# Performance work log

Hardware: AMD Instinct MI355X
Metric: run time of the kernel (lower is better)

Reference implementation:

```python
import jax, jax.numpy as jnp
import numpy as np

B, T = 16, 8192
L, RC, DC, SC, EC, E, NC = 16, 32, 32, 256, 256, 100, 256


def conv1d(x, w, b, dilation=1):
    # x: [B, Cin, T], w: [Cout, Cin, K], b: [Cout]
    y = jax.lax.conv_general_dilated(
        x, w, window_strides=(1,), padding='VALID',
        rhs_dilation=(dilation,), dimension_numbers=('NCH', 'OIH', 'NCH'))
    return y + b[None, :, None]


def setup_inputs() -> dict:
    key = jax.random.key(0)
    ks = jax.random.split(key, 32)
    n = lambda k, shp: (jax.random.normal(k, shp) * 0.1).astype(jnp.float32)
    return dict(
        tokens=jax.random.randint(ks[0], (B, T), 0, NC),
        emb=n(ks[1], (NC, E)),
        init_w=n(ks[2], (RC, E, 1)), init_b=n(ks[3], (RC,)),
        dil_w=n(ks[4], (L, DC, RC, 2)), dil_b=n(ks[5], (L, DC)),
        filt_w=n(ks[6], (L, DC, DC, 2)), filt_b=n(ks[7], (L, DC)),
        gate_w=n(ks[8], (L, DC, DC, 2)), gate_b=n(ks[9], (L, DC)),
        res_w=n(ks[10], (L, RC, DC, 1)), res_b=n(ks[11], (L, RC)),
        skip_w=n(ks[12], (L, SC, DC, 1)), skip_b=n(ks[13], (L, SC)),
        end1_w=n(ks[14], (EC, SC, 1)), end1_b=n(ks[15], (EC,)),
        end2_w=n(ks[16], (EC, EC, 1)), end2_b=n(ks[17], (EC,)),
        fc1_w=n(ks[18], (128, 256)), fc1_b=n(ks[19], (128,)),
        fc2_w=n(ks[20], (128, 128)), fc2_b=n(ks[21], (128,)),
        fc3_w=n(ks[22], (64, 128)), fc3_b=n(ks[23], (64,)),
        fc4_w=n(ks[24], (NC, 64)), fc4_b=n(ks[25], (NC,)),
    )


def reference(tokens, emb, init_w, init_b, dil_w, dil_b, filt_w, filt_b,
              gate_w, gate_b, res_w, res_b, skip_w, skip_b,
              end1_w, end1_b, end2_w, end2_b,
              fc1_w, fc1_b, fc2_w, fc2_b, fc3_w, fc3_b, fc4_w, fc4_b):
    x = emb[tokens]                     # [B, T, E]
    x = jnp.transpose(x, (0, 2, 1))     # [B, E, T]
    x = conv1d(x, init_w, init_b)       # [B, RC, T]
    skip = None
    for i in range(L):
        d = 2 ** (i % 4)                # dilation resets each block of 4 layers
        xp = jnp.pad(x, ((0, 0), (0, 0), (d + 1, 0)))        # left pad d+1
        residual = conv1d(xp, dil_w[i], dil_b[i], dilation=d)  # [B, DC, T+1]
        f = jnp.tanh(conv1d(residual, filt_w[i], filt_b[i]))   # [B, DC, T]
        g = jax.nn.sigmoid(conv1d(residual, gate_w[i], gate_b[i]))
        x = f * g
        skip = conv1d(x, skip_w[i], skip_b[i])   # overwritten each layer (source bug, kept faithful)
        x = conv1d(x, res_w[i], res_b[i]) + residual[:, :, :-1]
    h = jax.nn.relu(conv1d(jax.nn.relu(skip), end1_w, end1_b))
    h = conv1d(h, end2_w, end2_b)       # [B, EC, T]
    h = h[:, :, -1]                     # [B, 256] last timestep only
    h = jax.nn.relu(h @ fc1_w.T + fc1_b)
    h = jax.nn.relu(h @ fc2_w.T + fc2_b)
    h = jax.nn.relu(h @ fc3_w.T + fc3_b)
    out = h @ fc4_w.T + fc4_b           # [B, NC]
    return out
```

## Files before the change

### kernel.cpp

```cpp
#include <hip/hip_runtime.h>


#define BB 16
#define TT 8192
#define LL 16
#define W0 77
#define NT 256

typedef __attribute__((ext_vector_type(8)))  short short8;
typedef __attribute__((ext_vector_type(16))) float float16;

#define MFMA_B16(a, b, c) __builtin_amdgcn_mfma_f32_32x32x16_bf16(a, b, c, 0, 0, 0)

__device__ __forceinline__ short f2bs(float f) {
  union { float ff; unsigned u; } v; v.ff = f;
  unsigned u = v.u;
  return (short)((u + 0x7FFFu + ((u >> 16) & 1u)) >> 16);
}
__device__ __forceinline__ float b2f(short h) {
  union { unsigned u; float f; } v;
  v.u = ((unsigned)(unsigned short)h) << 16; return v.f;
}
__device__ __forceinline__ float fast_sigmoid(float x) {
  return 1.f / (1.f + __expf(-x));
}
__device__ __forceinline__ float fast_tanh(float x) {
  return 2.f / (1.f + __expf(-2.f * x)) - 1.f;
}

__device__ __forceinline__ void bfrag2(const float* w, int n, int kh, short8* out) {
  #pragma unroll
  for (int h = 0; h < 2; h++) {
    short8 v;
    #pragma unroll
    for (int j = 0; j < 8; j++) v[j] = f2bs(w[(16 * h + kh * 8 + j) * 32 + n]);
    out[h] = v;
  }
}
__device__ __forceinline__ void afrag2(const short* src, int row, int kh, short8* out) {
  #pragma unroll
  for (int h = 0; h < 2; h++)
    out[h] = *(const short8*)&src[row * 32 + 16 * h + 8 * kh];
}

__global__ __launch_bounds__(NT) void wavenet_kernel(
    const int* __restrict__ tokens,
    const float* __restrict__ emb,
    const float* __restrict__ init_w, const float* __restrict__ init_b,
    const float* __restrict__ dil_w,  const float* __restrict__ dil_b,
    const float* __restrict__ filt_w, const float* __restrict__ filt_b,
    const float* __restrict__ gate_w, const float* __restrict__ gate_b,
    const float* __restrict__ res_w,  const float* __restrict__ res_b,
    const float* __restrict__ skip_w, const float* __restrict__ skip_b,
    const float* __restrict__ end1_w, const float* __restrict__ end1_b,
    const float* __restrict__ end2_w, const float* __restrict__ end2_b,
    const float* __restrict__ fc1_w,  const float* __restrict__ fc1_b,
    const float* __restrict__ fc2_w,  const float* __restrict__ fc2_b,
    const float* __restrict__ fc3_w,  const float* __restrict__ fc3_b,
    const float* __restrict__ fc4_w,  const float* __restrict__ fc4_b,
    float* __restrict__ out)
{
  __shared__ float wts[7 * 1024];
  __shared__ float bias[4 * 32];
  __shared__ float resbuf[76 * 32];
  __shared__ __align__(16) short xbuf_bf[W0 * 32];
  __shared__ __align__(16) short resbuf_bf[76 * 32];
  __shared__ __align__(16) short xmid_bf[76 * 32];
  __shared__ int   tok[W0];
  __shared__ float vecA[256], vecB[256];

  const int b   = blockIdx.x;
  const int tid = threadIdx.x;
  const int lane = tid & 63;
  const int wv   = tid >> 6;
  const int m    = lane & 31;
  const int kh   = lane >> 5;
  const int g    = tid >> 5;

  float pw[7][4];
  float pb[4];

  if (tid < W0) tok[tid] = tokens[b * TT + (TT - 1 - tid)];
  for (int idx = tid; idx < 100 * 32; idx += NT) {
    int e = idx >> 5, cc = idx & 31;
    wts[idx] = init_w[cc * 100 + e];
  }
  if (tid < 32) bias[tid] = init_b[tid];

  #pragma unroll
  for (int j = 0; j < 4; j++) {
    int idx = tid + j * NT;
    int rc = idx >> 5, cc = idx & 31;
    int base = cc * 32 + rc;
    pw[0][j] = dil_w[base * 2 + 0];
    pw[1][j] = dil_w[base * 2 + 1];
    pw[2][j] = filt_w[base * 2 + 0];
    pw[3][j] = filt_w[base * 2 + 1];
    pw[4][j] = gate_w[base * 2 + 0];
    pw[5][j] = gate_w[base * 2 + 1];
    pw[6][j] = res_w[base];
  }
  if (tid < 32) {
    pb[0] = dil_b[tid]; pb[1] = filt_b[tid];
    pb[2] = gate_b[tid]; pb[3] = res_b[tid];
  }
  __syncthreads();

  {
    const int c = tid & 31;
    const float bc = bias[c];
    for (int base0 = 0; base0 < W0; base0 += 32) {
      float acc[4] = {bc, bc, bc, bc};
      const float* er[4];
      #pragma unroll
      for (int j = 0; j < 4; j++) {
        int u = base0 + g + 8 * j; if (u > W0 - 1) u = W0 - 1;
        er[j] = emb + tok[u] * 100;
      }
      #pragma unroll 5
      for (int eq = 0; eq < 100; eq += 4) {
        float w0 = wts[(eq+0)*32+c], w1 = wts[(eq+1)*32+c];
        float w2 = wts[(eq+2)*32+c], w3 = wts[(eq+3)*32+c];
        #pragma unroll
        for (int j = 0; j < 4; j++) {
          float4 e4 = *(const float4*)(er[j] + eq);
          acc[j] += (w0 * e4.x + w1 * e4.y) + (w2 * e4.z + w3 * e4.w);
        }
      }
      #pragma unroll
      for (int j = 0; j < 4; j++) {
        int u = base0 + g + 8 * j;
        if (u < W0) xbuf_bf[u * 32 + c] = f2bs(acc[j]);
      }
    }
  }
  __syncthreads();

  int Win = W0;
  for (int i = 0; i < LL; i++) {
    const int d = 1 << (i & 3);
    const int Wout = Win - d - 1;
    const int T1 = (Wout + 1 + 31) >> 5;
    const int T2 = (Wout + 31) >> 5;

    #pragma unroll
    for (int j = 0; j < 4; j++) {
      int idx = tid + j * NT;
      wts[idx]        = pw[0][j];
      wts[1024 + idx] = pw[1][j];
      wts[2048 + idx] = pw[2][j];
      wts[3072 + idx] = pw[3][j];
      wts[4096 + idx] = pw[4][j];
      wts[5120 + idx] = pw[5][j];
      wts[6144 + idx] = pw[6][j];
    }
    if (tid < 32) {
      bias[tid]      = pb[0];
      bias[32 + tid] = pb[1];
      bias[64 + tid] = pb[2];
      bias[96 + tid] = pb[3];
    }
    __syncthreads();

    if (i + 1 < LL) {
      const int ii = i + 1;
      #pragma unroll
      for (int j = 0; j < 4; j++) {
        int idx = tid + j * NT;
        int rc = idx >> 5, cc = idx & 31;
        int base = (ii * 32 + cc) * 32 + rc;
        pw[0][j] = dil_w[base * 2 + 0];
        pw[1][j] = dil_w[base * 2 + 1];
        pw[2][j] = filt_w[base * 2 + 0];
        pw[3][j] = filt_w[base * 2 + 1];
        pw[4][j] = gate_w[base * 2 + 0];
        pw[5][j] = gate_w[base * 2 + 1];
        pw[6][j] = res_w[base];
      }
      if (tid < 32) {
        pb[0] = dil_b[ii * 32 + tid]; pb[1] = filt_b[ii * 32 + tid];
        pb[2] = gate_b[ii * 32 + tid]; pb[3] = res_b[ii * 32 + tid];
      }
    }

    if (wv < T1) {
      const int R = wv * 32;
      short8 bD0[2], bD1[2];
      bfrag2(wts,        m, kh, bD0);
      bfrag2(wts + 1024, m, kh, bD1);
      int vra = R + m + d; if (vra > Win - 1) vra = Win - 1;
      int vrz = R + m;     if (vrz > Win - 1) vrz = Win - 1;
      short8 aA[2], aZ[2];
      afrag2(xbuf_bf, vra, kh, aA);
      afrag2(xbuf_bf, vrz, kh, aZ);
      float16 acc;
      const float bc = bias[m];
      #pragma unroll
      for (int r = 0; r < 16; r++) acc[r] = bc;
      acc = MFMA_B16(aA[0], bD0[0], acc);
      acc = MFMA_B16(aA[1], bD0[1], acc);
      acc = MFMA_B16(aZ[0], bD1[0], acc);
      acc = MFMA_B16(aZ[1], bD1[1], acc);
      #pragma unroll
      for (int r = 0; r < 16; r++) {
        int row = (r & 3) + 8 * (r >> 2) + 4 * kh;
        int vr = R + row;
        if (vr <= Wout) {
          resbuf[vr * 32 + m]    = acc[r];
          resbuf_bf[vr * 32 + m] = f2bs(acc[r]);
        }
      }
    }
    __syncthreads();

    if (wv < T2) {
      const int R = wv * 32;
      short8 bF0[2], bF1[2], bG0[2], bG1[2];
      bfrag2(wts + 2048, m, kh, bF0);
      bfrag2(wts + 3072, m, kh, bF1);
      bfrag2(wts + 4096, m, kh, bG0);
      bfrag2(wts + 5120, m, kh, bG1);
      int r1 = R + m + 1; if (r1 > Wout) r1 = Wout;
      int r0 = R + m;     if (r0 > Wout) r0 = Wout;
      short8 a1[2], a0[2];
      afrag2(resbuf_bf, r1, kh, a1);
      afrag2(resbuf_bf, r0, kh, a0);
      float16 accF, accG;
      const float bf = bias[32 + m], bg = bias[64 + m];
      #pragma unroll
      for (int r = 0; r < 16; r++) { accF[r] = bf; accG[r] = bg; }
      accF = MFMA_B16(a1[0], bF0[0], accF);
      accF = MFMA_B16(a1[1], bF0[1], accF);
      accF = MFMA_B16(a0[0], bF1[0], accF);
      accF = MFMA_B16(a0[1], bF1[1], accF);
      accG = MFMA_B16(a1[0], bG0[0], accG);
      accG = MFMA_B16(a1[1], bG0[1], accG);
      accG = MFMA_B16(a0[0], bG1[0], accG);
      accG = MFMA_B16(a0[1], bG1[1], accG);
      #pragma unroll
      for (int r = 0; r < 16; r++) {
        int row = (r & 3) + 8 * (r >> 2) + 4 * kh;
        int uf = R + row;
        if (uf < Wout)
          xmid_bf[uf * 32 + m] = f2bs(fast_tanh(accF[r]) * fast_sigmoid(accG[r]));
      }
      asm volatile("s_waitcnt lgkmcnt(0)" ::: "memory");

      short8 bR[2];
      bfrag2(wts + 6144, m, kh, bR);
      int rx = R + m; if (rx > Wout - 1) rx = Wout - 1;
      short8 aX[2];
      afrag2(xmid_bf, rx, kh, aX);
      float16 accX;
      const float br = bias[96 + m];
      #pragma unroll
      for (int r = 0; r < 16; r++) {
        int row = (r & 3) + 8 * (r >> 2) + 4 * kh;
        int rr = R + row + 1; if (rr > Wout) rr = Wout;
        accX[r] = br + resbuf[rr * 32 + m];
      }
      accX = MFMA_B16(aX[0], bR[0], accX);
      accX = MFMA_B16(aX[1], bR[1], accX);
      #pragma unroll
      for (int r = 0; r < 16; r++) {
        int row = (r & 3) + 8 * (r >> 2) + 4 * kh;
        int uf = R + row;
        if (uf < Wout) xbuf_bf[uf * 32 + m] = f2bs(accX[r]);
      }
    }
    __syncthreads();
    Win = Wout;
  }

  {
    float acc = skip_b[15 * 256 + tid];
    const float* wr = skip_w + (15 * 256 + tid) * 32;
    #pragma unroll
    for (int k = 0; k < 32; k += 4) {
      float4 w = *(const float4*)&wr[k];
      acc += (w.x * b2f(xmid_bf[k])   + w.y * b2f(xmid_bf[k+1]))
           + (w.z * b2f(xmid_bf[k+2]) + w.w * b2f(xmid_bf[k+3]));
    }
    vecA[tid] = fmaxf(acc, 0.f);
  }
  __syncthreads();
  {
    const float* wr = end1_w + tid * 256;
    float a4[4] = {0.f, 0.f, 0.f, 0.f};
    #pragma unroll 4
    for (int k = 0; k < 256; k += 16) {
      #pragma unroll
      for (int q = 0; q < 4; q++) {
        float4 w = *(const float4*)&wr[k + 4 * q];
        a4[q] += (w.x * vecA[k+4*q] + w.y * vecA[k+4*q+1]) + (w.z * vecA[k+4*q+2] + w.w * vecA[k+4*q+3]);
      }
    }
    vecB[tid] = fmaxf(end1_b[tid] + (a4[0] + a4[1]) + (a4[2] + a4[3]), 0.f);
  }
  __syncthreads();
  {
    const float* wr = end2_w + tid * 256;
    float a4[4] = {0.f, 0.f, 0.f, 0.f};
    #pragma unroll 4
    for (int k = 0; k < 256; k += 16) {
      #pragma unroll
      for (int q = 0; q < 4; q++) {
        float4 w = *(const float4*)&wr[k + 4 * q];
        a4[q] += (w.x * vecB[k+4*q] + w.y * vecB[k+4*q+1]) + (w.z * vecB[k+4*q+2] + w.w * vecB[k+4*q+3]);
      }
    }
    vecA[tid] = end2_b[tid] + (a4[0] + a4[1]) + (a4[2] + a4[3]);
  }
  __syncthreads();
  if (tid < 128) {
    const float* wr = fc1_w + tid * 256;
    float a4[4] = {0.f, 0.f, 0.f, 0.f};
    #pragma unroll 4
    for (int k = 0; k < 256; k += 16) {
      #pragma unroll
      for (int q = 0; q < 4; q++) {
        float4 w = *(const float4*)&wr[k + 4 * q];
        a4[q] += (w.x * vecA[k+4*q] + w.y * vecA[k+4*q+1]) + (w.z * vecA[k+4*q+2] + w.w * vecA[k+4*q+3]);
      }
    }
    vecB[tid] = fmaxf(fc1_b[tid] + (a4[0] + a4[1]) + (a4[2] + a4[3]), 0.f);
  }
  __syncthreads();
  if (tid < 128) {
    const float* wr = fc2_w + tid * 128;
    float a4[4] = {0.f, 0.f, 0.f, 0.f};
    #pragma unroll 2
    for (int k = 0; k < 128; k += 16) {
      #pragma unroll
      for (int q = 0; q < 4; q++) {
        float4 w = *(const float4*)&wr[k + 4 * q];
        a4[q] += (w.x * vecB[k+4*q] + w.y * vecB[k+4*q+1]) + (w.z * vecB[k+4*q+2] + w.w * vecB[k+4*q+3]);
      }
    }
    vecA[tid] = fmaxf(fc2_b[tid] + (a4[0] + a4[1]) + (a4[2] + a4[3]), 0.f);
  }
  __syncthreads();
  if (tid < 64) {
    const float* wr = fc3_w + tid * 128;
    float a4[4] = {0.f, 0.f, 0.f, 0.f};
    #pragma unroll 2
    for (int k = 0; k < 128; k += 16) {
      #pragma unroll
      for (int q = 0; q < 4; q++) {
        float4 w = *(const float4*)&wr[k + 4 * q];
        a4[q] += (w.x * vecA[k+4*q] + w.y * vecA[k+4*q+1]) + (w.z * vecA[k+4*q+2] + w.w * vecA[k+4*q+3]);
      }
    }
    vecB[tid] = fmaxf(fc3_b[tid] + (a4[0] + a4[1]) + (a4[2] + a4[3]), 0.f);
  }
  __syncthreads();
  {
    const float* wr = fc4_w + tid * 64;
    float a4[4] = {0.f, 0.f, 0.f, 0.f};
    #pragma unroll
    for (int k = 0; k < 64; k += 16) {
      #pragma unroll
      for (int q = 0; q < 4; q++) {
        float4 w = *(const float4*)&wr[k + 4 * q];
        a4[q] += (w.x * vecB[k+4*q] + w.y * vecB[k+4*q+1]) + (w.z * vecB[k+4*q+2] + w.w * vecB[k+4*q+3]);
      }
    }
    out[b * 256 + tid] = fc4_b[tid] + (a4[0] + a4[1]) + (a4[2] + a4[3]);
  }
}

extern "C" void kernel_launch(void* const* d_in, const int* in_sizes, int n_in,
                              void* d_out, int out_size, void* d_ws, size_t ws_size,
                              hipStream_t stream) {
  wavenet_kernel<<<BB, NT, 0, stream>>>(
      (const int*)d_in[0],    (const float*)d_in[1],  (const float*)d_in[2],  (const float*)d_in[3],
      (const float*)d_in[4],  (const float*)d_in[5],  (const float*)d_in[6],  (const float*)d_in[7],
      (const float*)d_in[8],  (const float*)d_in[9],  (const float*)d_in[10], (const float*)d_in[11],
      (const float*)d_in[12], (const float*)d_in[13], (const float*)d_in[14], (const float*)d_in[15],
      (const float*)d_in[16], (const float*)d_in[17], (const float*)d_in[18], (const float*)d_in[19],
      (const float*)d_in[20], (const float*)d_in[21], (const float*)d_in[22], (const float*)d_in[23],
      (const float*)d_in[24], (const float*)d_in[25], (float*)d_out);
}
```

Baseline: 240.0 us.

## Double-buffer pre-converted bf16 weight fragments in LDS, drop per-layer barrier

```diff
diff --git a/kernel.cpp b/kernel.cpp
--- a/kernel.cpp
+++ b/kernel.cpp
@@ -28,19 +28,15 @@
   return 2.f / (1.f + __expf(-2.f * x)) - 1.f;
 }
 
-__device__ __forceinline__ void bfrag2(const float* w, int n, int kh, short8* out) {
-  #pragma unroll
-  for (int h = 0; h < 2; h++) {
-    short8 v;
-    #pragma unroll
-    for (int j = 0; j < 8; j++) v[j] = f2bs(w[(16 * h + kh * 8 + j) * 32 + n]);
-    out[h] = v;
-  }
-}
 __device__ __forceinline__ void afrag2(const short* src, int row, int kh, short8* out) {
   #pragma unroll
   for (int h = 0; h < 2; h++)
     out[h] = *(const short8*)&src[row * 32 + 16 * h + 8 * kh];
+}
+__device__ __forceinline__ void bfragL(const short* bw, int mat, int n, int kh, short8* out) {
+  #pragma unroll
+  for (int h = 0; h < 2; h++)
+    out[h] = *(const short8*)&bw[((mat * 2 + h) * 64 + n * 2 + kh) * 8];
 }
 
 __global__ __launch_bounds__(NT) void wavenet_kernel(
@@ -60,8 +56,8 @@
     const float* __restrict__ fc4_w,  const float* __restrict__ fc4_b,
     float* __restrict__ out)
 {
-  __shared__ float wts[7 * 1024];
-  __shared__ float bias[4 * 32];
+  __shared__ __align__(16) short bfw[2][7168];
+  __shared__ float bias2[2][128];
   __shared__ float resbuf[76 * 32];
   __shared__ __align__(16) short xbuf_bf[W0 * 32];
   __shared__ __align__(16) short resbuf_bf[76 * 32];
@@ -69,36 +65,38 @@
   __shared__ int   tok[W0];
   __shared__ float vecA[256], vecB[256];
 
-  const int b   = blockIdx.x;
-  const int tid = threadIdx.x;
+  const int b    = blockIdx.x;
+  const int tid  = threadIdx.x;
   const int lane = tid & 63;
   const int wv   = tid >> 6;
   const int m    = lane & 31;
   const int kh   = lane >> 5;
   const int g    = tid >> 5;
+  const int cc   = tid & 31;
 
   float pw[7][4];
   float pb[4];
 
+  float* iwT = (float*)&bfw[1][0];
+
   if (tid < W0) tok[tid] = tokens[b * TT + (TT - 1 - tid)];
   for (int idx = tid; idx < 100 * 32; idx += NT) {
-    int e = idx >> 5, cc = idx & 31;
-    wts[idx] = init_w[cc * 100 + e];
-  }
-  if (tid < 32) bias[tid] = init_b[tid];
+    int e = idx >> 5, c2 = idx & 31;
+    iwT[idx] = init_w[c2 * 100 + e];
+  }
+  if (tid < 32) vecA[tid] = init_b[tid];
 
   #pragma unroll
-  for (int j = 0; j < 4; j++) {
-    int idx = tid + j * NT;
-    int rc = idx >> 5, cc = idx & 31;
+  for (int q = 0; q < 4; q++) {
+    int rc = g + 8 * q;
     int base = cc * 32 + rc;
-    pw[0][j] = dil_w[base * 2 + 0];
-    pw[1][j] = dil_w[base * 2 + 1];
-    pw[2][j] = filt_w[base * 2 + 0];
-    pw[3][j] = filt_w[base * 2 + 1];
-    pw[4][j] = gate_w[base * 2 + 0];
-    pw[5][j] = gate_w[base * 2 + 1];
-    pw[6][j] = res_w[base];
+    pw[0][q] = dil_w[base * 2 + 0];
+    pw[1][q] = dil_w[base * 2 + 1];
+    pw[2][q] = filt_w[base * 2 + 0];
+    pw[3][q] = filt_w[base * 2 + 1];
+    pw[4][q] = gate_w[base * 2 + 0];
+    pw[5][q] = gate_w[base * 2 + 1];
+    pw[6][q] = res_w[base];
   }
   if (tid < 32) {
     pb[0] = dil_b[tid]; pb[1] = filt_b[tid];
@@ -107,8 +105,7 @@
   __syncthreads();
 
   {
-    const int c = tid & 31;
-    const float bc = bias[c];
+    const float bc = vecA[cc];
     for (int base0 = 0; base0 < W0; base0 += 32) {
       float acc[4] = {bc, bc, bc, bc};
       const float* er[4];
@@ -119,8 +116,8 @@
       }
       #pragma unroll 5
       for (int eq = 0; eq < 100; eq += 4) {
-        float w0 = wts[(eq+0)*32+c], w1 = wts[(eq+1)*32+c];
-        float w2 = wts[(eq+2)*32+c], w3 = wts[(eq+3)*32+c];
+        float w0 = iwT[(eq+0)*32+cc], w1 = iwT[(eq+1)*32+cc];
+        float w2 = iwT[(eq+2)*32+cc], w3 = iwT[(eq+3)*32+cc];
         #pragma unroll
         for (int j = 0; j < 4; j++) {
           float4 e4 = *(const float4*)(er[j] + eq);
@@ -130,9 +127,18 @@
       #pragma unroll
       for (int j = 0; j < 4; j++) {
         int u = base0 + g + 8 * j;
-        if (u < W0) xbuf_bf[u * 32 + c] = f2bs(acc[j]);
-      }
-    }
+        if (u < W0) xbuf_bf[u * 32 + cc] = f2bs(acc[j]);
+      }
+    }
+  }
+  #pragma unroll
+  for (int mat = 0; mat < 7; mat++)
+    #pragma unroll
+    for (int q = 0; q < 4; q++)
+      bfw[0][((mat * 2 + (q >> 1)) * 64 + cc * 2 + (q & 1)) * 8 + g] = f2bs(pw[mat][q]);
+  if (tid < 32) {
+    bias2[0][tid] = pb[0]; bias2[0][32+tid] = pb[1];
+    bias2[0][64+tid] = pb[2]; bias2[0][96+tid] = pb[3];
   }
   __syncthreads();
 
@@ -140,42 +146,24 @@
   for (int i = 0; i < LL; i++) {
     const int d = 1 << (i & 3);
     const int Wout = Win - d - 1;
-    const int T1 = (Wout + 1 + 31) >> 5;
+    const int T1 = (Wout + 32) >> 5;
     const int T2 = (Wout + 31) >> 5;
-
-    #pragma unroll
-    for (int j = 0; j < 4; j++) {
-      int idx = tid + j * NT;
-      wts[idx]        = pw[0][j];
-      wts[1024 + idx] = pw[1][j];
-      wts[2048 + idx] = pw[2][j];
-      wts[3072 + idx] = pw[3][j];
-      wts[4096 + idx] = pw[4][j];
-      wts[5120 + idx] = pw[5][j];
-      wts[6144 + idx] = pw[6][j];
-    }
-    if (tid < 32) {
-      bias[tid]      = pb[0];
-      bias[32 + tid] = pb[1];
-      bias[64 + tid] = pb[2];
-      bias[96 + tid] = pb[3];
-    }
-    __syncthreads();
+    const short* bw = bfw[i & 1];
+    const float* bs = bias2[i & 1];
 
     if (i + 1 < LL) {
       const int ii = i + 1;
       #pragma unroll
-      for (int j = 0; j < 4; j++) {
-        int idx = tid + j * NT;
-        int rc = idx >> 5, cc = idx & 31;
+      for (int q = 0; q < 4; q++) {
+        int rc = g + 8 * q;
         int base = (ii * 32 + cc) * 32 + rc;
-        pw[0][j] = dil_w[base * 2 + 0];
-        pw[1][j] = dil_w[base * 2 + 1];
-        pw[2][j] = filt_w[base * 2 + 0];
-        pw[3][j] = filt_w[base * 2 + 1];
-        pw[4][j] = gate_w[base * 2 + 0];
-        pw[5][j] = gate_w[base * 2 + 1];
-        pw[6][j] = res_w[base];
+        pw[0][q] = dil_w[base * 2 + 0];
+        pw[1][q] = dil_w[base * 2 + 1];
+        pw[2][q] = filt_w[base * 2 + 0];
+        pw[3][q] = filt_w[base * 2 + 1];
+        pw[4][q] = gate_w[base * 2 + 0];
+        pw[5][q] = gate_w[base * 2 + 1];
+        pw[6][q] = res_w[base];
       }
       if (tid < 32) {
         pb[0] = dil_b[ii * 32 + tid]; pb[1] = filt_b[ii * 32 + tid];
@@ -186,15 +174,15 @@
     if (wv < T1) {
       const int R = wv * 32;
       short8 bD0[2], bD1[2];
-      bfrag2(wts,        m, kh, bD0);
-      bfrag2(wts + 1024, m, kh, bD1);
+      bfragL(bw, 0, m, kh, bD0);
+      bfragL(bw, 1, m, kh, bD1);
       int vra = R + m + d; if (vra > Win - 1) vra = Win - 1;
       int vrz = R + m;     if (vrz > Win - 1) vrz = Win - 1;
       short8 aA[2], aZ[2];
       afrag2(xbuf_bf, vra, kh, aA);
       afrag2(xbuf_bf, vrz, kh, aZ);
       float16 acc;
-      const float bc = bias[m];
+      const float bc = bs[m];
       #pragma unroll
       for (int r = 0; r < 16; r++) acc[r] = bc;
       acc = MFMA_B16(aA[0], bD0[0], acc);
@@ -216,17 +204,17 @@
     if (wv < T2) {
       const int R = wv * 32;
       short8 bF0[2], bF1[2], bG0[2], bG1[2];
-      bfrag2(wts + 2048, m, kh, bF0);
-      bfrag2(wts + 3072, m, kh, bF1);
-      bfrag2(wts + 4096, m, kh, bG0);
-      bfrag2(wts + 5120, m, kh, bG1);
+      bfragL(bw, 2, m, kh, bF0);
+      bfragL(bw, 3, m, kh, bF1);
+      bfragL(bw, 4, m, kh, bG0);
+      bfragL(bw, 5, m, kh, bG1);
       int r1 = R + m + 1; if (r1 > Wout) r1 = Wout;
       int r0 = R + m;     if (r0 > Wout) r0 = Wout;
       short8 a1[2], a0[2];
       afrag2(resbuf_bf, r1, kh, a1);
       afrag2(resbuf_bf, r0, kh, a0);
       float16 accF, accG;
-      const float bf = bias[32 + m], bg = bias[64 + m];
+      const float bf = bs[32 + m], bg = bs[64 + m];
       #pragma unroll
       for (int r = 0; r < 16; r++) { accF[r] = bf; accG[r] = bg; }
       accF = MFMA_B16(a1[0], bF0[0], accF);
@@ -247,12 +235,12 @@
       asm volatile("s_waitcnt lgkmcnt(0)" ::: "memory");
 
       short8 bR[2];
-      bfrag2(wts + 6144, m, kh, bR);
+      bfragL(bw, 6, m, kh, bR);
       int rx = R + m; if (rx > Wout - 1) rx = Wout - 1;
       short8 aX[2];
       afrag2(xmid_bf, rx, kh, aX);
       float16 accX;
-      const float br = bias[96 + m];
+      const float br = bs[96 + m];
       #pragma unroll
       for (int r = 0; r < 16; r++) {
         int row = (r & 3) + 8 * (r >> 2) + 4 * kh;
@@ -266,6 +254,19 @@
         int row = (r & 3) + 8 * (r >> 2) + 4 * kh;
         int uf = R + row;
         if (uf < Wout) xbuf_bf[uf * 32 + m] = f2bs(accX[r]);
+      }
+    }
+
+    if (i + 1 < LL) {
+      short* bwN = bfw[(i + 1) & 1];
+      #pragma unroll
+      for (int mat = 0; mat < 7; mat++)
+        #pragma unroll
+        for (int q = 0; q < 4; q++)
+          bwN[((mat * 2 + (q >> 1)) * 64 + cc * 2 + (q & 1)) * 8 + g] = f2bs(pw[mat][q]);
+      if (tid < 32) {
+        float* bN = bias2[(i + 1) & 1];
+        bN[tid] = pb[0]; bN[32+tid] = pb[1]; bN[64+tid] = pb[2]; bN[96+tid] = pb[3];
       }
     }
     __syncthreads();
```

Result: faster. 216.7 us (-9.7%).
